# Optimization experiments

Measured on AMD Instinct MI355X. Metric: run time of the kernel, lower is better.

The kernel has to match this reference:

```python
import jax, jax.numpy as jnp
import numpy as np

D_MODEL = 1024
N_HEADS = 16
D_K = D_MODEL // N_HEADS
THETA = 10000.0
BATCH = 1
SEQ = 4096


def setup_inputs() -> dict:
    key = jax.random.key(0)
    ks = jax.random.split(key, 5)
    std = (2.0 / (D_MODEL + D_MODEL)) ** 0.5
    mk = lambda k: jax.random.truncated_normal(k, -3.0, 3.0, (D_MODEL, D_MODEL), jnp.float32) * std
    return {
        "x": jax.random.normal(ks[0], (BATCH, SEQ, D_MODEL), jnp.float32),
        "Wq": mk(ks[1]),
        "Wk": mk(ks[2]),
        "Wv": mk(ks[3]),
        "Wo": mk(ks[4]),
    }


def _rope(x, pos, inv_freq):
    # x: [b, h, s, d_k]; pos: [s]; inv_freq: [d_k/2]
    angles = pos[:, None].astype(jnp.float32) * inv_freq  # [s, d_k/2]
    cos = jnp.repeat(jnp.cos(angles), 2, axis=-1)  # [s, d_k]
    sin = jnp.repeat(jnp.sin(angles), 2, axis=-1)
    # interleaved rotation: (-x1, x0, -x3, x2, ...)
    x_rot = jnp.stack([-x[..., 1::2], x[..., 0::2]], axis=-1).reshape(x.shape)
    return x * cos + x_rot * sin


def reference(x, Wq, Wk, Wv, Wo):
    b, s, _ = x.shape
    h, dk = N_HEADS, D_K
    proj = lambda W: jnp.einsum('bsi,oi->bso', x, W).reshape(b, s, h, dk).transpose(0, 2, 1, 3)
    q = proj(Wq)
    k = proj(Wk)
    v = proj(Wv)
    pos = jnp.arange(s)
    inv_freq = 1.0 / THETA ** (jnp.arange(0, dk, 2, dtype=jnp.float32) / dk)
    q = _rope(q, pos, inv_freq)
    k = _rope(k, pos, inv_freq)
    scores = jnp.einsum('bhqd,bhkd->bhqk', q, k) / jnp.sqrt(jnp.asarray(dk, jnp.float32))
    causal_mask = jnp.arange(s)[None, :] > jnp.arange(s)[:, None]  # [s, s], True above diag
    scores = jnp.where(causal_mask, -jnp.inf, scores)
    weights = jax.nn.softmax(scores, axis=-1)
    out = jnp.einsum('bhqk,bhkd->bhqd', weights, v)
    out = out.transpose(0, 2, 1, 3).reshape(b, s, h * dk)
    return jnp.einsum('bsi,oi->bso', out, Wo)
```

## Files before the change

### kernel.cpp

```cpp
#include <hip/hip_runtime.h>
#include <hip/hip_bf16.h>


typedef __hip_bfloat16 bf16;
using s16x4 = __attribute__((ext_vector_type(4))) short;
using s16x8 = __attribute__((ext_vector_type(8))) short;
using f32x4 = __attribute__((ext_vector_type(4))) float;

#define SEQ 4096
#define DMODEL 1024
#define NHEADS 16
#define DK 64
#define LOG2_THETA 13.287712379549449f
#define SCALE_LOG2E 0.1803368801111244f

#if defined(__has_builtin)
#if __has_builtin(__builtin_amdgcn_mfma_f32_16x16x16bf16_1k)
#define HAVE_MFMA16 1
#endif
#endif

__device__ __forceinline__ f32x4 mfma16(s16x4 a, s16x4 b, f32x4 c) {
#ifdef HAVE_MFMA16
  return __builtin_amdgcn_mfma_f32_16x16x16bf16_1k(a, b, c, 0, 0, 0);
#else
  asm volatile("v_mfma_f32_16x16x16_bf16 %0, %1, %2, %0"
               : "+v"(c) : "v"(a), "v"(b));
  return c;
#endif
}

__device__ __forceinline__ void async16(const bf16* g, bf16* l) {
  __builtin_amdgcn_global_load_lds(
      (const __attribute__((address_space(1))) unsigned int*)g,
      (__attribute__((address_space(3))) unsigned int*)l, 16, 0, 0);
}

__global__ __launch_bounds__(256)
void conv_kernel(const float* __restrict__ s0, const float* __restrict__ s1,
                 const float* __restrict__ s2, const float* __restrict__ s3,
                 const float* __restrict__ s4,
                 bf16* __restrict__ d0, bf16* __restrict__ d1,
                 bf16* __restrict__ d2, bf16* __restrict__ d3,
                 bf16* __restrict__ d4) {
  const int z = blockIdx.z;
  const float* s = (z == 0) ? s0 : (z == 1) ? s1 : (z == 2) ? s2 : (z == 3) ? s3 : s4;
  bf16* d = (z == 0) ? d0 : (z == 1) ? d1 : (z == 2) ? d2 : (z == 3) ? d3 : d4;
  const int n = (z == 0) ? SEQ * DMODEL : DMODEL * DMODEL;
  for (int i = (blockIdx.x * 256 + threadIdx.x) * 8; i < n; i += 512 * 256 * 8) {
    const float4 a = *(const float4*)(s + i);
    const float4 b = *(const float4*)(s + i + 4);
    union { bf16 h[8]; s16x8 v; } u;
    u.h[0] = __float2bfloat16(a.x); u.h[1] = __float2bfloat16(a.y);
    u.h[2] = __float2bfloat16(a.z); u.h[3] = __float2bfloat16(a.w);
    u.h[4] = __float2bfloat16(b.x); u.h[5] = __float2bfloat16(b.y);
    u.h[6] = __float2bfloat16(b.z); u.h[7] = __float2bfloat16(b.w);
    *(s16x8*)(d + i) = u.v;
  }
}

__global__ __launch_bounds__(256)
void gemm_kernel(const bf16* __restrict__ A,
                 const bf16* __restrict__ W0, const bf16* __restrict__ W1,
                 const bf16* __restrict__ W2,
                 bf16* __restrict__ D0, bf16* __restrict__ D1,
                 bf16* __restrict__ D2) {
  const int mode = (int)blockIdx.z;
  const bf16* __restrict__ W = (mode == 1) ? W1 : (mode == 2) ? W2 : W0;
  bf16* __restrict__ D = (mode == 1) ? D1 : (mode == 2) ? D2 : D0;

  const int tid  = threadIdx.x;
  const int lane = tid & 63;
  const int wave = tid >> 6;
  const int wm = wave >> 1, wn = wave & 1;
  const int quad = lane >> 4, l16 = lane & 15;
  const int m0 = blockIdx.x * 128;
  const int n0 = blockIdx.y * 128;

  __shared__ __align__(16) char gsm[49152];
  bf16* const smem = (bf16*)gsm;

  f32x4 acc[4][4] = {};

  const int ldrow = lane >> 2;
  const int ldcol = (lane & 3) * 8;

  auto stage = [&](int b, int k0) {
#pragma unroll
    for (int c = 0; c < 2; ++c) {
      const int chunk = wave * 2 + c;
      const int row = chunk * 16 + ldrow;
      async16(&A[(size_t)(m0 + row) * DMODEL + k0 + ldcol],
              &smem[b * 8192 + chunk * 512]);
      async16(&W[(size_t)(n0 + row) * DMODEL + k0 + ldcol],
              &smem[b * 8192 + 4096 + chunk * 512]);
    }
  };

  stage(0, 0);
  __syncthreads();

  for (int t = 0; t < 32; ++t) {
    const int cur = t & 1;
    if (t < 31) stage(cur ^ 1, (t + 1) * 32);

    s16x8 af[4], bfr[4];
#pragma unroll
    for (int i = 0; i < 4; ++i)
      af[i] = *(const s16x8*)&smem[cur * 8192 + (wm * 64 + i * 16 + l16) * 32 + quad * 8];
#pragma unroll
    for (int j = 0; j < 4; ++j)
      bfr[j] = *(const s16x8*)&smem[cur * 8192 + 4096 + (wn * 64 + j * 16 + l16) * 32 + quad * 8];
#pragma unroll
    for (int i = 0; i < 4; ++i)
#pragma unroll
      for (int j = 0; j < 4; ++j)
        acc[i][j] = __builtin_amdgcn_mfma_f32_16x16x32_bf16(af[i], bfr[j],
                                                            acc[i][j], 0, 0, 0);
    __syncthreads();
  }

  bf16* const Esw = (bf16*)(gsm + 16384) + wave * 4096;

  if (mode == 2) {
#pragma unroll
    for (int i = 0; i < 4; ++i)
#pragma unroll
      for (int j = 0; j < 4; ++j)
#pragma unroll
        for (int r = 0; r < 4; ++r)
          Esw[(j * 16 + l16) * 64 + i * 16 + quad * 4 + r] =
              __float2bfloat16(acc[i][j][r]);
  } else {
#pragma unroll
    for (int i = 0; i < 4; ++i)
#pragma unroll
      for (int j = 0; j < 4; ++j)
#pragma unroll
        for (int r = 0; r < 4; ++r)
          Esw[(i * 16 + quad * 4 + r) * 64 + j * 16 + l16] =
              __float2bfloat16(acc[i][j][r]);
  }
  __syncthreads();

  const int h = (n0 >> 6) + wn;
  const int g  = lane >> 3;
  const int c8 = (lane & 7) * 8;

  if (mode == 2) {
#pragma unroll
    for (int t = 0; t < 8; ++t) {
      const int d = t * 8 + g;
      const s16x8 v = *(const s16x8*)&Esw[d * 64 + c8];
      *(s16x8*)&D[((size_t)h * DK + d) * SEQ + m0 + wm * 64 + c8] = v;
    }
  } else {
    const float qs = (mode == 0) ? SCALE_LOG2E : 1.0f;
    float sn[4], cs[4], s8[4], c8r[4], invf[4];
    const int srow0 = m0 + wm * 64 + g;
#pragma unroll
    for (int k = 0; k < 4; ++k) {
      const int p = (c8 >> 1) + k;
      invf[k] = __builtin_amdgcn_exp2f((float)p * (-2.0f / 64.0f) * LOG2_THETA);
      sincosf((float)srow0 * invf[k], &sn[k], &cs[k]);
      sincosf(8.0f * invf[k], &s8[k], &c8r[k]);
      sn[k] *= qs; cs[k] *= qs;
    }
#pragma unroll
    for (int t = 0; t < 8; ++t) {
      const int rl = t * 8 + g;
      union { bf16 h[8]; s16x8 v; } u, o;
      u.v = *(const s16x8*)&Esw[rl * 64 + c8];
#pragma unroll
      for (int k = 0; k < 4; ++k) {
        const float x0 = __bfloat162float(u.h[2 * k]);
        const float x1 = __bfloat162float(u.h[2 * k + 1]);
        o.h[2 * k]     = __float2bfloat16(x0 * cs[k] - x1 * sn[k]);
        o.h[2 * k + 1] = __float2bfloat16(x1 * cs[k] + x0 * sn[k]);
        const float ns_ = sn[k] * c8r[k] + cs[k] * s8[k];
        cs[k] = cs[k] * c8r[k] - sn[k] * s8[k];
        sn[k] = ns_;
      }
      const int srow = m0 + wm * 64 + rl;
      *(s16x8*)&D[((size_t)h * SEQ + srow) * DK + c8] = o.v;
    }
  }
}

__global__ __launch_bounds__(256)
void gemmo_kernel(const bf16* __restrict__ A, const bf16* __restrict__ W,
                  float* __restrict__ Df) {
  const int tid  = threadIdx.x;
  const int lane = tid & 63;
  const int wave = tid >> 6;
  const int wm = wave >> 1, wn = wave & 1;
  const int quad = lane >> 4, l16 = lane & 15;
  const int m0 = blockIdx.x * 64;
  const int n0 = blockIdx.y * 128;

  __shared__ __align__(16) bf16 sm[2][6144];

  f32x4 acc[2][4] = {};
  const int ldrow = lane >> 2;
  const int ldcol = (lane & 3) * 8;

  auto stage = [&](int b, int k0) {
    {
      const int row = wave * 16 + ldrow;
      async16(&A[(size_t)(m0 + row) * DMODEL + k0 + ldcol], &sm[b][wave * 512]);
    }
#pragma unroll
    for (int c = 0; c < 2; ++c) {
      const int row = (wave * 2 + c) * 16 + ldrow;
      async16(&W[(size_t)(n0 + row) * DMODEL + k0 + ldcol],
              &sm[b][2048 + (wave * 2 + c) * 512]);
    }
  };

  stage(0, 0);
  __syncthreads();

  for (int t = 0; t < 32; ++t) {
    const int cur = t & 1;
    if (t < 31) stage(cur ^ 1, (t + 1) * 32);

    s16x8 af[2], bfr[4];
#pragma unroll
    for (int i = 0; i < 2; ++i)
      af[i] = *(const s16x8*)&sm[cur][(wm * 32 + i * 16 + l16) * 32 + quad * 8];
#pragma unroll
    for (int j = 0; j < 4; ++j)
      bfr[j] = *(const s16x8*)&sm[cur][2048 + (wn * 64 + j * 16 + l16) * 32 + quad * 8];
#pragma unroll
    for (int i = 0; i < 2; ++i)
#pragma unroll
      for (int j = 0; j < 4; ++j)
        acc[i][j] = __builtin_amdgcn_mfma_f32_16x16x32_bf16(af[i], bfr[j],
                                                            acc[i][j], 0, 0, 0);
    __syncthreads();
  }

#pragma unroll
  for (int i = 0; i < 2; ++i)
#pragma unroll
    for (int j = 0; j < 4; ++j) {
      const int col = n0 + wn * 64 + j * 16 + l16;
#pragma unroll
      for (int r = 0; r < 4; ++r) {
        const int srow = m0 + wm * 32 + i * 16 + quad * 4 + r;
        Df[(size_t)srow * DMODEL + col] = acc[i][j][r];
      }
    }
}

__global__ __launch_bounds__(256, 4)
void attn_kernel(const bf16* __restrict__ Q, const bf16* __restrict__ K,
                 const bf16* __restrict__ Vt, bf16* __restrict__ O) {
  const int tid  = threadIdx.x;
  const int lane = tid & 63;
  const int wave = tid >> 6;
  const int quad = lane >> 4, l16 = lane & 15;
  const int wq = wave & 1;
  const int wk = wave >> 1;

  const int i  = (int)blockIdx.x;
  const int j  = i & 255;
  const int vv = 3 - (i >> 8);
  const int h  = j & 15;
  const int a  = j >> 4;
  const int qb = vv * 16 + ((vv & 1) ? (15 - a) : a);

  const bf16* __restrict__ Qh = Q + (size_t)h * SEQ * DK;
  const bf16* __restrict__ Kh = K + (size_t)h * SEQ * DK;
  const bf16* __restrict__ Vh = Vt + (size_t)h * DK * SEQ;

  __shared__ __align__(16) char smemb[32768];
  bf16* __restrict__ smem = (bf16*)smemb;
  bf16* __restrict__ KsB = smem;
  bf16* __restrict__ VsB = smem + 8192;

  const int srow = lane >> 3;
  const int schk = (lane & 7) ^ srow;
  const int xsw  = l16 & 7;

  const int q0 = qb * 64;
  const int qw = q0 + wq * 32;
  const int nb = qb + 1;

  const short ONE = 0x3F80;
  const s16x4 ones4 = {ONE, ONE, ONE, ONE};

  s16x8 aq[2][2];
#pragma unroll
  for (int gq = 0; gq < 2; ++gq) {
    const size_t qr = (size_t)(qw + gq * 16 + l16) * DK;
    aq[gq][0] = *(const s16x8*)&Qh[qr + quad * 8];
    aq[gq][1] = *(const s16x8*)&Qh[qr + 32 + quad * 8];
  }

  f32x4 oacc[2][4] = {};
  f32x4 lacc[2] = {};

  {
#pragma unroll
    for (int c = 0; c < 2; ++c) {
      const int chunk = wave * 2 + c;
      async16(Kh + (size_t)(chunk * 8 + srow) * 64 + schk * 8,
              &KsB[chunk * 512]);
      async16(Vh + (size_t)(chunk * 8 + srow) * SEQ + schk * 8,
              &VsB[chunk * 512]);
    }
  }
  __syncthreads();

  for (int kb = 0; kb < nb; ++kb) {
    const int cur = kb & 1;
    if (kb + 1 < nb) {
      const int nxt = cur ^ 1;
      const int kv1 = (kb + 1) * 64;
      const bf16* kg = Kh + (size_t)kv1 * DK;
#pragma unroll
      for (int c = 0; c < 2; ++c) {
        const int chunk = wave * 2 + c;
        async16(kg + (size_t)(chunk * 8 + srow) * 64 + schk * 8,
                &KsB[nxt * 4096 + chunk * 512]);
        async16(Vh + (size_t)(chunk * 8 + srow) * SEQ + kv1 + schk * 8,
                &VsB[nxt * 4096 + chunk * 512]);
      }
    }

    const bf16* __restrict__ Ksc = &KsB[cur * 4096];
    const bf16* __restrict__ Vsc = &VsB[cur * 4096];

    f32x4 sc[2][2] = {};
    __builtin_amdgcn_s_setprio(1);
#pragma unroll
    for (int hh = 0; hh < 2; ++hh) {
      const bf16* kr = &Ksc[(wk * 32 + hh * 16 + l16) * 64];
      const s16x8 ak0 = *(const s16x8*)&kr[(quad ^ xsw) * 8];
      const s16x8 ak1 = *(const s16x8*)&kr[((quad + 4) ^ xsw) * 8];
#pragma unroll
      for (int gq = 0; gq < 2; ++gq) {
        sc[gq][hh] = __builtin_amdgcn_mfma_f32_16x16x32_bf16(ak0, aq[gq][0], sc[gq][hh], 0, 0, 0);
        sc[gq][hh] = __builtin_amdgcn_mfma_f32_16x16x32_bf16(ak1, aq[gq][1], sc[gq][hh], 0, 0, 0);
      }
    }
    __builtin_amdgcn_s_setprio(0);

    if (kb == nb - 1) {
#pragma unroll
      for (int gq = 0; gq < 2; ++gq) {
        const int lim = wq * 32 + gq * 16 + l16 - wk * 32 - quad * 4;
#pragma unroll
        for (int hh = 0; hh < 2; ++hh)
#pragma unroll
          for (int r = 0; r < 4; ++r)
            if (hh * 16 + r > lim) sc[gq][hh][r] = -1e30f;
      }
    }

    s16x4 ap[2][2];
#pragma unroll
    for (int gq = 0; gq < 2; ++gq)
#pragma unroll
      for (int hh = 0; hh < 2; ++hh) {
        union { bf16 b[4]; s16x4 v; } pk;
#pragma unroll
        for (int r = 0; r < 4; ++r)
          pk.b[r] = __float2bfloat16(__builtin_amdgcn_exp2f(sc[gq][hh][r]));
        ap[gq][hh] = pk.v;
      }

    __builtin_amdgcn_s_setprio(1);
#pragma unroll
    for (int hh = 0; hh < 2; ++hh) {
      const int cg = wk * 4 + hh * 2 + (quad >> 1);
      const int eo = ((cg ^ xsw) << 3) + (quad & 1) * 4;
#pragma unroll
      for (int ns = 0; ns < 4; ++ns) {
        const s16x4 bv = *(const s16x4*)&Vsc[(ns * 16 + l16) * 64 + eo];
#pragma unroll
        for (int gq = 0; gq < 2; ++gq)
          oacc[gq][ns] = mfma16(ap[gq][hh], bv, oacc[gq][ns]);
      }
    }
#pragma unroll
    for (int gq = 0; gq < 2; ++gq)
#pragma unroll
      for (int hh = 0; hh < 2; ++hh)
        lacc[gq] = mfma16(ap[gq][hh], ones4, lacc[gq]);
    __builtin_amdgcn_s_setprio(0);

    __syncthreads();
  }

  float* __restrict__ Ored = (float*)smemb;
  float* __restrict__ lred = (float*)(smemb + 16896);
  bf16*  __restrict__ Obuf = (bf16*)(smemb + 17408);

  if (wk == 0) {
    if (l16 == 0)
#pragma unroll
      for (int gq = 0; gq < 2; ++gq)
#pragma unroll
        for (int r = 0; r < 4; ++r)
          lred[wq * 32 + gq * 16 + quad * 4 + r] = lacc[gq][r];
  } else {
#pragma unroll
    for (int gq = 0; gq < 2; ++gq)
#pragma unroll
      for (int ns = 0; ns < 4; ++ns)
#pragma unroll
        for (int r = 0; r < 4; ++r)
          Ored[(wq * 32 + gq * 16 + quad * 4 + r) * 66 + ns * 16 + l16] =
              oacc[gq][ns][r];
  }
  __syncthreads();
  if (wk == 1 && l16 == 0) {
#pragma unroll
    for (int gq = 0; gq < 2; ++gq)
#pragma unroll
      for (int r = 0; r < 4; ++r)
        lred[wq * 32 + gq * 16 + quad * 4 + r] += lacc[gq][r];
  }
  __syncthreads();
  if (wk == 0) {
#pragma unroll
    for (int gq = 0; gq < 2; ++gq) {
      float rl[4];
#pragma unroll
      for (int r = 0; r < 4; ++r)
        rl[r] = __builtin_amdgcn_rcpf(lred[wq * 32 + gq * 16 + quad * 4 + r]);
#pragma unroll
      for (int ns = 0; ns < 4; ++ns)
#pragma unroll
        for (int r = 0; r < 4; ++r) {
          const int row = wq * 32 + gq * 16 + quad * 4 + r;
          const float v = oacc[gq][ns][r] + Ored[row * 66 + ns * 16 + l16];
          Obuf[row * 72 + ns * 16 + l16] = __float2bfloat16(v * rl[r]);
        }
    }
  }
  __syncthreads();
#pragma unroll
  for (int p = 0; p < 2; ++p) {
    const int row = p * 32 + (tid >> 3);
    const int c8 = (tid & 7) * 8;
    const s16x8 v = *(const s16x8*)&Obuf[row * 72 + c8];
    *(s16x8*)&O[(size_t)(q0 + row) * DMODEL + h * DK + c8] = v;
  }
}

extern "C" void kernel_launch(void* const* d_in, const int* in_sizes, int n_in,
                              void* d_out, int out_size, void* d_ws, size_t ws_size,
                              hipStream_t stream) {
  const float* x  = (const float*)d_in[0];
  const float* Wq = (const float*)d_in[1];
  const float* Wk = (const float*)d_in[2];
  const float* Wv = (const float*)d_in[3];
  const float* Wo = (const float*)d_in[4];
  float* out = (float*)d_out;

  bf16* ws = (bf16*)d_ws;
  bf16* xb   = ws;
  bf16* Wqb  = xb  + (size_t)SEQ * DMODEL;
  bf16* Wkb  = Wqb + (size_t)DMODEL * DMODEL;
  bf16* Wvb  = Wkb + (size_t)DMODEL * DMODEL;
  bf16* Wob  = Wvb + (size_t)DMODEL * DMODEL;
  bf16* Qb   = Wob + (size_t)DMODEL * DMODEL;
  bf16* Kb   = Qb  + (size_t)SEQ * DMODEL;
  bf16* Vtb  = Kb  + (size_t)SEQ * DMODEL;
  bf16* Attn = Vtb + (size_t)SEQ * DMODEL;

  conv_kernel<<<dim3(512, 1, 5), 256, 0, stream>>>(
      x, Wq, Wk, Wv, Wo, xb, Wqb, Wkb, Wvb, Wob);
  gemm_kernel<<<dim3(SEQ / 128, DMODEL / 128, 3), 256, 0, stream>>>(
      xb, Wqb, Wkb, Wvb, Qb, Kb, Vtb);
  attn_kernel<<<dim3(64 * NHEADS), 256, 0, stream>>>(Qb, Kb, Vtb, Attn);
  gemmo_kernel<<<dim3(SEQ / 64, DMODEL / 128), 256, 0, stream>>>(
      Attn, Wob, out);
}
```

Measured before the change: 187.1 us.

## Split attention into 32-row query tiles with 2-wave blocks and direct V loads

The attention kernel now uses 128-thread blocks that each handle a 32-row query tile, giving 2048 blocks in place of 1024 blocks of 64 rows. Blocks are mapped so each XCD serves two heads, with a zigzag ordering over query tiles to balance the causal work. V fragments are loaded straight from global memory into registers instead of being staged through LDS. A wave whose whole key half lies above the diagonal skips its last block, and shared memory is halved. The aim is better load balance, locality and occupancy, at the cost of uncoalesced strided V loads and more redundant K traffic per query row.

```diff
diff --git a/kernel.cpp b/kernel.cpp
--- a/kernel.cpp
+++ b/kernel.cpp
@@ -253,39 +253,35 @@
     }
 }
 
-__global__ __launch_bounds__(256, 4)
+__global__ __launch_bounds__(128, 4)
 void attn_kernel(const bf16* __restrict__ Q, const bf16* __restrict__ K,
                  const bf16* __restrict__ Vt, bf16* __restrict__ O) {
   const int tid  = threadIdx.x;
   const int lane = tid & 63;
   const int wave = tid >> 6;
   const int quad = lane >> 4, l16 = lane & 15;
-  const int wq = wave & 1;
-  const int wk = wave >> 1;
-
-  const int i  = (int)blockIdx.x;
-  const int j  = i & 255;
-  const int vv = 3 - (i >> 8);
-  const int h  = j & 15;
-  const int a  = j >> 4;
-  const int qb = vv * 16 + ((vv & 1) ? (15 - a) : a);
+  const int wk = wave;
+
+  const int i    = (int)blockIdx.x;
+  const int xcd  = i & 7;
+  const int slot = i >> 3;
+  const int h    = xcd * 2 + (slot & 1);
+  const int v    = slot >> 1;
+  const int qt   = (((v ^ (v >> 4)) & 1) ? (127 - v) : v);
 
   const bf16* __restrict__ Qh = Q + (size_t)h * SEQ * DK;
   const bf16* __restrict__ Kh = K + (size_t)h * SEQ * DK;
   const bf16* __restrict__ Vh = Vt + (size_t)h * DK * SEQ;
 
-  __shared__ __align__(16) char smemb[32768];
-  bf16* __restrict__ smem = (bf16*)smemb;
-  bf16* __restrict__ KsB = smem;
-  bf16* __restrict__ VsB = smem + 8192;
+  __shared__ __align__(16) char smemb[16384];
+  bf16* __restrict__ KsB = (bf16*)smemb;
 
   const int srow = lane >> 3;
   const int schk = (lane & 7) ^ srow;
   const int xsw  = l16 & 7;
 
-  const int q0 = qb * 64;
-  const int qw = q0 + wq * 32;
-  const int nb = qb + 1;
+  const int q0 = qt * 32;
+  const int nb = (qt >> 1) + 1;
 
   const short ONE = 0x3F80;
   const s16x4 ones4 = {ONE, ONE, ONE, ONE};
@@ -293,7 +289,7 @@
   s16x8 aq[2][2];
 #pragma unroll
   for (int gq = 0; gq < 2; ++gq) {
-    const size_t qr = (size_t)(qw + gq * 16 + l16) * DK;
+    const size_t qr = (size_t)(q0 + gq * 16 + l16) * DK;
     aq[gq][0] = *(const s16x8*)&Qh[qr + quad * 8];
     aq[gq][1] = *(const s16x8*)&Qh[qr + 32 + quad * 8];
   }
@@ -301,127 +297,115 @@
   f32x4 oacc[2][4] = {};
   f32x4 lacc[2] = {};
 
-  {
-#pragma unroll
-    for (int c = 0; c < 2; ++c) {
-      const int chunk = wave * 2 + c;
-      async16(Kh + (size_t)(chunk * 8 + srow) * 64 + schk * 8,
-              &KsB[chunk * 512]);
-      async16(Vh + (size_t)(chunk * 8 + srow) * SEQ + schk * 8,
-              &VsB[chunk * 512]);
-    }
-  }
+  auto stageK = [&](int buf, int kv0) {
+    const bf16* kg = Kh + (size_t)kv0 * DK;
+#pragma unroll
+    for (int c = 0; c < 4; ++c) {
+      const int chunk = wave * 4 + c;
+      async16(kg + (size_t)(chunk * 8 + srow) * 64 + schk * 8,
+              &KsB[buf * 4096 + chunk * 512]);
+    }
+  };
+
+  stageK(0, 0);
   __syncthreads();
 
   for (int kb = 0; kb < nb; ++kb) {
     const int cur = kb & 1;
-    if (kb + 1 < nb) {
-      const int nxt = cur ^ 1;
-      const int kv1 = (kb + 1) * 64;
-      const bf16* kg = Kh + (size_t)kv1 * DK;
-#pragma unroll
-      for (int c = 0; c < 2; ++c) {
-        const int chunk = wave * 2 + c;
-        async16(kg + (size_t)(chunk * 8 + srow) * 64 + schk * 8,
-                &KsB[nxt * 4096 + chunk * 512]);
-        async16(Vh + (size_t)(chunk * 8 + srow) * SEQ + kv1 + schk * 8,
-                &VsB[nxt * 4096 + chunk * 512]);
+    const int kv0 = kb * 64;
+
+    const bool full = (kb == nb - 1) && ((nb - 1) * 64 + wk * 32 > q0 + 31);
+
+    s16x4 bv[2][4];
+    if (!full) {
+#pragma unroll
+      for (int hh = 0; hh < 2; ++hh)
+#pragma unroll
+        for (int ns = 0; ns < 4; ++ns)
+          bv[hh][ns] = *(const s16x4*)&Vh[(size_t)(ns * 16 + l16) * SEQ +
+                                          kv0 + wk * 32 + hh * 16 + quad * 4];
+    }
+
+    if (kb + 1 < nb) stageK(cur ^ 1, kv0 + 64);
+
+    if (!full) {
+      const bf16* __restrict__ Ksc = &KsB[cur * 4096];
+
+      f32x4 sc[2][2] = {};
+      __builtin_amdgcn_s_setprio(1);
+#pragma unroll
+      for (int hh = 0; hh < 2; ++hh) {
+        const bf16* kr = &Ksc[(wk * 32 + hh * 16 + l16) * 64];
+        const s16x8 ak0 = *(const s16x8*)&kr[(quad ^ xsw) * 8];
+        const s16x8 ak1 = *(const s16x8*)&kr[((quad + 4) ^ xsw) * 8];
+#pragma unroll
+        for (int gq = 0; gq < 2; ++gq) {
+          sc[gq][hh] = __builtin_amdgcn_mfma_f32_16x16x32_bf16(ak0, aq[gq][0], sc[gq][hh], 0, 0, 0);
+          sc[gq][hh] = __builtin_amdgcn_mfma_f32_16x16x32_bf16(ak1, aq[gq][1], sc[gq][hh], 0, 0, 0);
+        }
       }
-    }
-
-    const bf16* __restrict__ Ksc = &KsB[cur * 4096];
-    const bf16* __restrict__ Vsc = &VsB[cur * 4096];
-
-    f32x4 sc[2][2] = {};
-    __builtin_amdgcn_s_setprio(1);
-#pragma unroll
-    for (int hh = 0; hh < 2; ++hh) {
-      const bf16* kr = &Ksc[(wk * 32 + hh * 16 + l16) * 64];
-      const s16x8 ak0 = *(const s16x8*)&kr[(quad ^ xsw) * 8];
-      const s16x8 ak1 = *(const s16x8*)&kr[((quad + 4) ^ xsw) * 8];
-#pragma unroll
-      for (int gq = 0; gq < 2; ++gq) {
-        sc[gq][hh] = __builtin_amdgcn_mfma_f32_16x16x32_bf16(ak0, aq[gq][0], sc[gq][hh], 0, 0, 0);
-        sc[gq][hh] = __builtin_amdgcn_mfma_f32_16x16x32_bf16(ak1, aq[gq][1], sc[gq][hh], 0, 0, 0);
+      __builtin_amdgcn_s_setprio(0);
+
+      if (kb == nb - 1) {
+#pragma unroll
+        for (int gq = 0; gq < 2; ++gq) {
+          const int lim = q0 + gq * 16 + l16 - (nb - 1) * 64 - wk * 32 - quad * 4;
+#pragma unroll
+          for (int hh = 0; hh < 2; ++hh)
+#pragma unroll
+            for (int r = 0; r < 4; ++r)
+              if (hh * 16 + r > lim) sc[gq][hh][r] = -1e30f;
+        }
       }
-    }
-    __builtin_amdgcn_s_setprio(0);
-
-    if (kb == nb - 1) {
-#pragma unroll
-      for (int gq = 0; gq < 2; ++gq) {
-        const int lim = wq * 32 + gq * 16 + l16 - wk * 32 - quad * 4;
+
+      s16x4 ap[2][2];
+#pragma unroll
+      for (int gq = 0; gq < 2; ++gq)
+#pragma unroll
+        for (int hh = 0; hh < 2; ++hh) {
+          union { bf16 b[4]; s16x4 v; } pk;
+#pragma unroll
+          for (int r = 0; r < 4; ++r)
+            pk.b[r] = __float2bfloat16(__builtin_amdgcn_exp2f(sc[gq][hh][r]));
+          ap[gq][hh] = pk.v;
+        }
+
+      __builtin_amdgcn_s_setprio(1);
+#pragma unroll
+      for (int hh = 0; hh < 2; ++hh)
+#pragma unroll
+        for (int ns = 0; ns < 4; ++ns)
+#pragma unroll
+          for (int gq = 0; gq < 2; ++gq)
+            oacc[gq][ns] = mfma16(ap[gq][hh], bv[hh][ns], oacc[gq][ns]);
+#pragma unroll
+      for (int gq = 0; gq < 2; ++gq)
 #pragma unroll
         for (int hh = 0; hh < 2; ++hh)
-#pragma unroll
-          for (int r = 0; r < 4; ++r)
-            if (hh * 16 + r > lim) sc[gq][hh][r] = -1e30f;
-      }
-    }
-
-    s16x4 ap[2][2];
-#pragma unroll
-    for (int gq = 0; gq < 2; ++gq)
-#pragma unroll
-      for (int hh = 0; hh < 2; ++hh) {
-        union { bf16 b[4]; s16x4 v; } pk;
+          lacc[gq] = mfma16(ap[gq][hh], ones4, lacc[gq]);
+      __builtin_amdgcn_s_setprio(0);
+    }
+
+    __syncthreads();
+  }
+
+  float* __restrict__ Ored = (float*)smemb;
+  float* __restrict__ lred = (float*)(smemb + 8448);
+  bf16*  __restrict__ Obuf = (bf16*)(smemb + 8704);
+
+  if (wk == 1) {
+#pragma unroll
+    for (int gq = 0; gq < 2; ++gq) {
+#pragma unroll
+      for (int ns = 0; ns < 4; ++ns)
 #pragma unroll
         for (int r = 0; r < 4; ++r)
-          pk.b[r] = __float2bfloat16(__builtin_amdgcn_exp2f(sc[gq][hh][r]));
-        ap[gq][hh] = pk.v;
-      }
-
-    __builtin_amdgcn_s_setprio(1);
-#pragma unroll
-    for (int hh = 0; hh < 2; ++hh) {
-      const int cg = wk * 4 + hh * 2 + (quad >> 1);
-      const int eo = ((cg ^ xsw) << 3) + (quad & 1) * 4;
-#pragma unroll
-      for (int ns = 0; ns < 4; ++ns) {
-        const s16x4 bv = *(const s16x4*)&Vsc[(ns * 16 + l16) * 64 + eo];
-#pragma unroll
-        for (int gq = 0; gq < 2; ++gq)
-          oacc[gq][ns] = mfma16(ap[gq][hh], bv, oacc[gq][ns]);
-      }
-    }
-#pragma unroll
-    for (int gq = 0; gq < 2; ++gq)
-#pragma unroll
-      for (int hh = 0; hh < 2; ++hh)
-        lacc[gq] = mfma16(ap[gq][hh], ones4, lacc[gq]);
-    __builtin_amdgcn_s_setprio(0);
-
-    __syncthreads();
-  }
-
-  float* __restrict__ Ored = (float*)smemb;
-  float* __restrict__ lred = (float*)(smemb + 16896);
-  bf16*  __restrict__ Obuf = (bf16*)(smemb + 17408);
-
-  if (wk == 0) {
-    if (l16 == 0)
-#pragma unroll
-      for (int gq = 0; gq < 2; ++gq)
+          Ored[(gq * 16 + quad * 4 + r) * 66 + ns * 16 + l16] = oacc[gq][ns][r];
+      if (l16 == 0)
 #pragma unroll
         for (int r = 0; r < 4; ++r)
-          lred[wq * 32 + gq * 16 + quad * 4 + r] = lacc[gq][r];
-  } else {
-#pragma unroll
-    for (int gq = 0; gq < 2; ++gq)
-#pragma unroll
-      for (int ns = 0; ns < 4; ++ns)
-#pragma unroll
-        for (int r = 0; r < 4; ++r)
-          Ored[(wq * 32 + gq * 16 + quad * 4 + r) * 66 + ns * 16 + l16] =
-              oacc[gq][ns][r];
-  }
-  __syncthreads();
-  if (wk == 1 && l16 == 0) {
-#pragma unroll
-    for (int gq = 0; gq < 2; ++gq)
-#pragma unroll
-      for (int r = 0; r < 4; ++r)
-        lred[wq * 32 + gq * 16 + quad * 4 + r] += lacc[gq][r];
+          lred[gq * 16 + quad * 4 + r] = lacc[gq][r];
+    }
   }
   __syncthreads();
   if (wk == 0) {
@@ -430,24 +414,24 @@
       float rl[4];
 #pragma unroll
       for (int r = 0; r < 4; ++r)
-        rl[r] = __builtin_amdgcn_rcpf(lred[wq * 32 + gq * 16 + quad * 4 + r]);
+        rl[r] = __builtin_amdgcn_rcpf(lred[gq * 16 + quad * 4 + r] + lacc[gq][r]);
 #pragma unroll
       for (int ns = 0; ns < 4; ++ns)
 #pragma unroll
         for (int r = 0; r < 4; ++r) {
-          const int row = wq * 32 + gq * 16 + quad * 4 + r;
-          const float v = oacc[gq][ns][r] + Ored[row * 66 + ns * 16 + l16];
-          Obuf[row * 72 + ns * 16 + l16] = __float2bfloat16(v * rl[r]);
+          const int row = gq * 16 + quad * 4 + r;
+          const float val = oacc[gq][ns][r] + Ored[row * 66 + ns * 16 + l16];
+          Obuf[row * 72 + ns * 16 + l16] = __float2bfloat16(val * rl[r]);
         }
     }
   }
   __syncthreads();
 #pragma unroll
   for (int p = 0; p < 2; ++p) {
-    const int row = p * 32 + (tid >> 3);
+    const int row = p * 16 + (tid >> 3);
     const int c8 = (tid & 7) * 8;
-    const s16x8 v = *(const s16x8*)&Obuf[row * 72 + c8];
-    *(s16x8*)&O[(size_t)(q0 + row) * DMODEL + h * DK + c8] = v;
+    const s16x8 vv = *(const s16x8*)&Obuf[row * 72 + c8];
+    *(s16x8*)&O[(size_t)(q0 + row) * DMODEL + h * DK + c8] = vv;
   }
 }
 
@@ -476,7 +460,7 @@
       x, Wq, Wk, Wv, Wo, xb, Wqb, Wkb, Wvb, Wob);
   gemm_kernel<<<dim3(SEQ / 128, DMODEL / 128, 3), 256, 0, stream>>>(
       xb, Wqb, Wkb, Wvb, Qb, Kb, Vtb);
-  attn_kernel<<<dim3(64 * NHEADS), 256, 0, stream>>>(Qb, Kb, Vtb, Attn);
+  attn_kernel<<<dim3(2048), 128, 0, stream>>>(Qb, Kb, Vtb, Attn);
   gemmo_kernel<<<dim3(SEQ / 64, DMODEL / 128), 256, 0, stream>>>(
       Attn, Wob, out);
 }
```

New measurement: 300.1 us. 1.6x slower.

## Triple-buffer K tiles with explicit vmcnt waits and merge epilogue reductions

Applied to the files above, without the earlier changes.

The attention kernel now keeps K tiles in a three-slot LDS ring staged two iterations ahead, while V stays double-buffered one iterations ahead. A full __syncthreads at the end of each KV step is replaced by a targeted s_waitcnt vmcnt plus s_barrier, so the next loads can stay in flight. The epilogue folds the row-sum reduction into one LDS exchange with one fewer barrier. LDS use per block grows from 32KB to 40KB, which may lower occupancy, and the vmcnt counts must match the number of outstanding loads exactly.

```diff
diff --git a/kernel.cpp b/kernel.cpp
--- a/kernel.cpp
+++ b/kernel.cpp
@@ -274,10 +274,9 @@
   const bf16* __restrict__ Kh = K + (size_t)h * SEQ * DK;
   const bf16* __restrict__ Vh = Vt + (size_t)h * DK * SEQ;
 
-  __shared__ __align__(16) char smemb[32768];
-  bf16* __restrict__ smem = (bf16*)smemb;
-  bf16* __restrict__ KsB = smem;
-  bf16* __restrict__ VsB = smem + 8192;
+  __shared__ __align__(16) char smemb[40960];
+  bf16* __restrict__ KsB = (bf16*)smemb;
+  bf16* __restrict__ VsB = (bf16*)(smemb + 24576);
 
   const int srow = lane >> 3;
   const int schk = (lane & 7) ^ srow;
@@ -301,36 +300,44 @@
   f32x4 oacc[2][4] = {};
   f32x4 lacc[2] = {};
 
-  {
+  auto stageK = [&](int buf, int kv0) {
+    const bf16* kg = Kh + (size_t)kv0 * DK;
 #pragma unroll
     for (int c = 0; c < 2; ++c) {
       const int chunk = wave * 2 + c;
-      async16(Kh + (size_t)(chunk * 8 + srow) * 64 + schk * 8,
-              &KsB[chunk * 512]);
-      async16(Vh + (size_t)(chunk * 8 + srow) * SEQ + schk * 8,
-              &VsB[chunk * 512]);
-    }
-  }
-  __syncthreads();
-
+      async16(kg + (size_t)(chunk * 8 + srow) * 64 + schk * 8,
+              &KsB[buf * 4096 + chunk * 512]);
+    }
+  };
+  auto stageV = [&](int buf, int kv0) {
+#pragma unroll
+    for (int c = 0; c < 2; ++c) {
+      const int chunk = wave * 2 + c;
+      async16(Vh + (size_t)(chunk * 8 + srow) * SEQ + kv0 + schk * 8,
+              &VsB[buf * 4096 + chunk * 512]);
+    }
+  };
+
+  stageV(0, 0);
+  stageK(0, 0);
+  if (nb > 1) {
+    stageK(1, 64);
+    asm volatile("s_waitcnt vmcnt(2)" ::: "memory");
+  } else {
+    asm volatile("s_waitcnt vmcnt(0)" ::: "memory");
+  }
+  __builtin_amdgcn_s_barrier();
+  __builtin_amdgcn_sched_barrier(0);
+
+  int kcur = 0;
   for (int kb = 0; kb < nb; ++kb) {
-    const int cur = kb & 1;
-    if (kb + 1 < nb) {
-      const int nxt = cur ^ 1;
-      const int kv1 = (kb + 1) * 64;
-      const bf16* kg = Kh + (size_t)kv1 * DK;
-#pragma unroll
-      for (int c = 0; c < 2; ++c) {
-        const int chunk = wave * 2 + c;
-        async16(kg + (size_t)(chunk * 8 + srow) * 64 + schk * 8,
-                &KsB[nxt * 4096 + chunk * 512]);
-        async16(Vh + (size_t)(chunk * 8 + srow) * SEQ + kv1 + schk * 8,
-                &VsB[nxt * 4096 + chunk * 512]);
-      }
-    }
-
-    const bf16* __restrict__ Ksc = &KsB[cur * 4096];
-    const bf16* __restrict__ Vsc = &VsB[cur * 4096];
+    const int vcur = kb & 1;
+    if (kb + 1 < nb) stageV(vcur ^ 1, (kb + 1) * 64);
+    const bool deep = (kb + 2 < nb);
+    if (deep) stageK(kcur == 0 ? 2 : kcur - 1, (kb + 2) * 64);
+
+    const bf16* __restrict__ Ksc = &KsB[kcur * 4096];
+    const bf16* __restrict__ Vsc = &VsB[vcur * 4096];
 
     f32x4 sc[2][2] = {};
     __builtin_amdgcn_s_setprio(1);
@@ -391,37 +398,31 @@
         lacc[gq] = mfma16(ap[gq][hh], ones4, lacc[gq]);
     __builtin_amdgcn_s_setprio(0);
 
-    __syncthreads();
+    if (deep) asm volatile("s_waitcnt vmcnt(2)" ::: "memory");
+    else      asm volatile("s_waitcnt vmcnt(0)" ::: "memory");
+    __builtin_amdgcn_s_barrier();
+    __builtin_amdgcn_sched_barrier(0);
+    kcur = (kcur == 2) ? 0 : kcur + 1;
   }
 
   float* __restrict__ Ored = (float*)smemb;
   float* __restrict__ lred = (float*)(smemb + 16896);
   bf16*  __restrict__ Obuf = (bf16*)(smemb + 17408);
 
-  if (wk == 0) {
-    if (l16 == 0)
-#pragma unroll
-      for (int gq = 0; gq < 2; ++gq)
-#pragma unroll
-        for (int r = 0; r < 4; ++r)
-          lred[wq * 32 + gq * 16 + quad * 4 + r] = lacc[gq][r];
-  } else {
-#pragma unroll
-    for (int gq = 0; gq < 2; ++gq)
+  if (wk == 1) {
+#pragma unroll
+    for (int gq = 0; gq < 2; ++gq) {
 #pragma unroll
       for (int ns = 0; ns < 4; ++ns)
 #pragma unroll
         for (int r = 0; r < 4; ++r)
           Ored[(wq * 32 + gq * 16 + quad * 4 + r) * 66 + ns * 16 + l16] =
               oacc[gq][ns][r];
-  }
-  __syncthreads();
-  if (wk == 1 && l16 == 0) {
-#pragma unroll
-    for (int gq = 0; gq < 2; ++gq)
-#pragma unroll
-      for (int r = 0; r < 4; ++r)
-        lred[wq * 32 + gq * 16 + quad * 4 + r] += lacc[gq][r];
+      if (l16 == 0)
+#pragma unroll
+        for (int r = 0; r < 4; ++r)
+          lred[wq * 32 + gq * 16 + quad * 4 + r] = lacc[gq][r];
+    }
   }
   __syncthreads();
   if (wk == 0) {
@@ -430,14 +431,15 @@
       float rl[4];
 #pragma unroll
       for (int r = 0; r < 4; ++r)
-        rl[r] = __builtin_amdgcn_rcpf(lred[wq * 32 + gq * 16 + quad * 4 + r]);
+        rl[r] = __builtin_amdgcn_rcpf(lred[wq * 32 + gq * 16 + quad * 4 + r] +
+                                      lacc[gq][r]);
 #pragma unroll
       for (int ns = 0; ns < 4; ++ns)
 #pragma unroll
         for (int r = 0; r < 4; ++r) {
           const int row = wq * 32 + gq * 16 + quad * 4 + r;
-          const float v = oacc[gq][ns][r] + Ored[row * 66 + ns * 16 + l16];
-          Obuf[row * 72 + ns * 16 + l16] = __float2bfloat16(v * rl[r]);
+          const float val = oacc[gq][ns][r] + Ored[row * 66 + ns * 16 + l16];
+          Obuf[row * 72 + ns * 16 + l16] = __float2bfloat16(val * rl[r]);
         }
     }
   }
```

Result: slower. 195.5 us (+4.5%).
